# Optimization experiments

Hardware: AMD Instinct MI355X
Metric: run time of the kernel (lower is better)

Reference implementation:

```python
import jax, jax.numpy as jnp
import numpy as np

ALIGNED_H, ALIGNED_W, ALIGNED_T = 7, 7, 4
SPATIAL_SCALE, TIME_SCALE = 1.0 / 16.0, 1.0
B, C, T, H, W = 4, 256, 16, 64, 64
N_ROIS = 1200


def setup_inputs() -> dict:
    key = jax.random.key(0)
    kf, kb, kx, ky, kw, kh, kt, kd = jax.random.split(key, 8)
    features = jax.random.normal(kf, (B, C, T, H, W), dtype=jnp.float32)
    b = jax.random.randint(kb, (N_ROIS,), 0, B).astype(jnp.float32)
    # image-space boxes (1024x1024 image, stride-16 features); temporal interval in frame units
    x1 = jax.random.uniform(kx, (N_ROIS,), minval=0.0, maxval=700.0)
    y1 = jax.random.uniform(ky, (N_ROIS,), minval=0.0, maxval=700.0)
    x2 = jnp.minimum(x1 + jax.random.uniform(kw, (N_ROIS,), minval=32.0, maxval=320.0), 1023.0)
    y2 = jnp.minimum(y1 + jax.random.uniform(kh, (N_ROIS,), minval=32.0, maxval=320.0), 1023.0)
    t1 = jax.random.uniform(kt, (N_ROIS,), minval=0.0, maxval=10.0)
    t2 = jnp.minimum(t1 + jax.random.uniform(kd, (N_ROIS,), minval=2.0, maxval=6.0), 15.0)
    rois = jnp.stack([b, x1, y1, x2, y2, t1, t2], axis=1)  # [N, 7]
    return {"features": features, "rois": rois}


def _axis_samples(start, end, size, n_out):
    # classic roi_align sampling: bin = (end - start + 1) / (n_out - 1), sample at start + i*bin
    length = jnp.maximum(end - start + 1.0, 1.0)                                  # [N]
    step = length / (n_out - 1.0)
    coord = start[:, None] + step[:, None] * jnp.arange(n_out, dtype=jnp.float32)[None, :]  # [N, n_out]
    valid = (coord >= 0.0) & (coord < size)
    lo = jnp.clip(jnp.floor(coord), 0.0, size - 1.0)
    frac = coord - lo
    lo_i = lo.astype(jnp.int32)
    hi_i = jnp.minimum(lo_i + 1, size - 1)
    return lo_i, hi_i, frac, valid.astype(jnp.float32)


def roi_align_3d(features, rois, p_t, p_h, p_w, sscale, tscale):
    Bf, Cf, Tf, Hf, Wf = features.shape
    f = jnp.transpose(features, (0, 2, 3, 4, 1))  # [B,T,H,W,C] channel-last for clean gather
    bidx = rois[:, 0].astype(jnp.int32)
    x1 = rois[:, 1] * sscale
    y1 = rois[:, 2] * sscale
    x2 = rois[:, 3] * sscale
    y2 = rois[:, 4] * sscale
    t1 = rois[:, 5] * tscale
    t2 = rois[:, 6] * tscale
    tl, th, tfr, tv = _axis_samples(t1, t2, Tf, p_t)  # [N, p_t]
    yl, yh, yfr, yv = _axis_samples(y1, y2, Hf, p_h)  # [N, p_h]
    xl, xh, xfr, xv = _axis_samples(x1, x2, Wf, p_w)  # [N, p_w]
    b4 = bidx[:, None, None, None]
    out = jnp.zeros((rois.shape[0], p_t, p_h, p_w, Cf), dtype=features.dtype)
    # trilinear interpolation: sum over 8 corners
    for ti, wt in ((tl, 1.0 - tfr), (th, tfr)):
        for yi, wy in ((yl, 1.0 - yfr), (yh, yfr)):
            for xi, wx in ((xl, 1.0 - xfr), (xh, xfr)):
                v = f[b4, ti[:, :, None, None], yi[:, None, :, None], xi[:, None, None, :]]  # [N,pt,ph,pw,C]
                w = wt[:, :, None, None] * wy[:, None, :, None] * wx[:, None, None, :]
                out = out + v * w[..., None]
    # zero out-of-bounds sample points (matches CUDA kernel behavior)
    mask = tv[:, :, None, None] * yv[:, None, :, None] * xv[:, None, None, :]
    out = out * mask[..., None]
    return jnp.transpose(out, (0, 4, 1, 2, 3))  # [N, C, p_t, p_h, p_w]


def _avg_pool3d_k2s1(x):
    s = x[..., :-1, :, :] + x[..., 1:, :, :]
    s = s[..., :, :-1, :] + s[..., :, 1:, :]
    s = s[..., :, :, :-1] + s[..., :, :, 1:]
    return s * 0.125


def reference(features, rois):
    x = roi_align_3d(features, rois, ALIGNED_T + 1, ALIGNED_H + 1, ALIGNED_W + 1,
                     SPATIAL_SCALE, TIME_SCALE)
    return _avg_pool3d_k2s1(x)  # [N, C, ALIGNED_T, ALIGNED_H, ALIGNED_W]
```

## Files before the change

### kernel.cpp

```cpp
#include <hip/hip_runtime.h>

#define C_ 256
#define T_ 16
#define H_ 64
#define W_ 64
#define PT 5
#define PH 8
#define PW 8
#define OT 4
#define OH 7
#define OW 7
#define SSCALE (1.0f/16.0f)
#define TSCALE 1.0f
#define CG 32
#define LROW 66
#define NOUT (CG * OT * OH * OW)

typedef float f4v __attribute__((ext_vector_type(4)));
typedef float f2v __attribute__((ext_vector_type(2)));
typedef _Float16 h4v __attribute__((ext_vector_type(4)));
typedef _Float16 h8v __attribute__((ext_vector_type(8)));

__global__ __launch_bounds__(256) void transpose_kernel(const float* __restrict__ f,
                                                        _Float16* __restrict__ ft) {
    __shared__ _Float16 tile[64][260];
    const int THW = T_ * H_ * W_;
    int thw0 = blockIdx.x * 64;
    int b = blockIdx.y;

    int l4 = threadIdx.x & 15;
    int cr = threadIdx.x >> 4;
#pragma unroll 4
    for (int k = 0; k < 16; ++k) {
        int c = k * 16 + cr;
        const f4v* src = reinterpret_cast<const f4v*>(
            &f[((size_t)b * C_ + c) * THW + thw0 + l4 * 4]);
        f4v v = __builtin_nontemporal_load(src);
        tile[l4 * 4 + 0][c] = (_Float16)v[0];
        tile[l4 * 4 + 1][c] = (_Float16)v[1];
        tile[l4 * 4 + 2][c] = (_Float16)v[2];
        tile[l4 * 4 + 3][c] = (_Float16)v[3];
    }
    __syncthreads();

    int wv = threadIdx.x >> 6;
    int ln = threadIdx.x & 63;
    size_t orow = ((size_t)b * THW + thw0) * C_;
#pragma unroll
    for (int i = 0; i < 16; ++i) {
        int t = wv * 16 + i;
        h4v v = *reinterpret_cast<const h4v*>(&tile[t][ln * 4]);
        *reinterpret_cast<h4v*>(&ft[orow + (size_t)t * C_ + ln * 4]) = v;
    }
}

__global__ __launch_bounds__(256) void roi_kernel(const _Float16* __restrict__ ft,
                                                  const float* __restrict__ rois,
                                                  float* __restrict__ out) {
    __shared__ float scratch[NOUT];
    __shared__ float sroi[7];
    __shared__ int2 s_trow[PT]; __shared__ float2 s_twt[PT];
    __shared__ int2 s_yrow[PH]; __shared__ float2 s_ywt[PH];
    __shared__ int2 s_xoff[PW]; __shared__ float2 s_xwt[PW];

    int bid = blockIdx.x;
    int r = bid >> 3;
    int cg = bid & 7;
    int c0 = cg * CG;

    if (threadIdx.x < 7) sroi[threadIdx.x] = rois[r * 7 + threadIdx.x];
    __syncthreads();

    if (threadIdx.x < 21) {
        int i = threadIdx.x;
        float start, end, size;
        int j, n, scale;
        if (i < 5) {
            j = i; n = PT;
            start = sroi[5] * TSCALE; end = sroi[6] * TSCALE;
            size = (float)T_; scale = H_ * W_ * C_ * 2;
        } else if (i < 13) {
            j = i - 5; n = PH;
            start = sroi[2] * SSCALE; end = sroi[4] * SSCALE;
            size = (float)H_; scale = W_ * C_ * 2;
        } else {
            j = i - 13; n = PW;
            start = sroi[1] * SSCALE; end = sroi[3] * SSCALE;
            size = (float)W_; scale = C_ * 2;
        }
        float length = fmaxf(end - start + 1.0f, 1.0f);
        float step = length / (float)(n - 1);
        float coord = start + step * (float)j;
        float valid = (coord >= 0.0f && coord < size) ? 1.0f : 0.0f;
        float lo = fminf(fmaxf(floorf(coord), 0.0f), size - 1.0f);
        int lo_i = (int)lo;
        int hi_i = min(lo_i + 1, (int)size - 1);
        float fr = coord - lo;
        int2 offs; offs.x = lo_i * scale; offs.y = hi_i * scale;
        float2 wts; wts.x = (1.0f - fr) * valid; wts.y = fr * valid;
        if (i < 5)       { s_trow[j] = offs; s_twt[j] = wts; }
        else if (i < 13) { s_yrow[j] = offs; s_ywt[j] = wts; }
        else             { s_xoff[j] = offs; s_xwt[j] = wts; }
    }
    __syncthreads();

    int b = (int)sroi[0];
    int c4 = threadIdx.x & 3;
    int slot = threadIdx.x >> 2;
    const char* fb = (const char*)ft
        + ((size_t)b * (T_ * H_ * W_ * C_) + (size_t)(c0 + c4 * 8)) * 2;

    float (*buf)[LROW] = (float(*)[LROW])scratch;
    int cc = threadIdx.x & 31;
    int hh = threadIdx.x >> 5;

    float racc[OT][OW];
#pragma unroll
    for (int t = 0; t < OT; ++t)
#pragma unroll
        for (int w = 0; w < OW; ++w) racc[t][w] = 0.0f;

    int y = slot >> 3, x = slot & 7;
    int2 yr = s_yrow[y]; float2 yw = s_ywt[y];
    int2 xo = s_xoff[x]; float2 xw = s_xwt[x];

#pragma unroll
    for (int t = 0; t < PT; ++t) {
        if (t) __syncthreads();

        int2 tr = s_trow[t];
        float2 tw = s_twt[t];
        int rA = tr.x + yr.x;
        int rB = tr.x + yr.y;
        int rC = tr.y + yr.x;
        int rD = tr.y + yr.y;
        float wA = tw.x * yw.x, wB = tw.x * yw.y;
        float wC = tw.y * yw.x, wD = tw.y * yw.y;

        f4v accL = {0.f, 0.f, 0.f, 0.f};
        f4v accH = {0.f, 0.f, 0.f, 0.f};
#pragma unroll
        for (int tap = 0; tap < 8; ++tap) {
            int ro = (tap & 1) ? ((tap >> 1) == 0 ? rA : (tap >> 1) == 1 ? rB
                                  : (tap >> 1) == 2 ? rC : rD) + xo.y
                               : ((tap >> 1) == 0 ? rA : (tap >> 1) == 1 ? rB
                                  : (tap >> 1) == 2 ? rC : rD) + xo.x;
            float w = ((tap >> 1) == 0 ? wA : (tap >> 1) == 1 ? wB
                       : (tap >> 1) == 2 ? wC : wD) * ((tap & 1) ? xw.y : xw.x);
            h8v h = *(const h8v*)(fb + ro);
            f4v lo = {(float)h[0], (float)h[1], (float)h[2], (float)h[3]};
            f4v hi = {(float)h[4], (float)h[5], (float)h[6], (float)h[7]};
            accL += w * lo;
            accH += w * hi;
        }
        {
            float* col = &buf[c4 * 8][slot];
            col[0 * LROW] = accL[0];
            col[1 * LROW] = accL[1];
            col[2 * LROW] = accL[2];
            col[3 * LROW] = accL[3];
            col[4 * LROW] = accH[0];
            col[5 * LROW] = accH[1];
            col[6 * LROW] = accH[2];
            col[7 * LROW] = accH[3];
        }
        __syncthreads();

        if (hh < 7) {
            const float* p = &buf[cc][hh * 8];
            float p2[8];
#pragma unroll
            for (int x2 = 0; x2 < 4; ++x2) {
                f2v a = *(const f2v*)(p + 2 * x2);
                f2v bq = *(const f2v*)(p + 8 + 2 * x2);
                f2v s = a + bq;
                p2[2 * x2] = s[0];
                p2[2 * x2 + 1] = s[1];
            }
#pragma unroll
            for (int w = 0; w < OW; ++w) {
                float pw = p2[w] + p2[w + 1];
                if (t < OT) racc[t][w] += pw;
                if (t > 0) racc[t - 1][w] += pw;
            }
        }
    }
    __syncthreads();

    if (hh < 7) {
        int base = cc * (OT * OH * OW) + hh * OW;
#pragma unroll
        for (int t = 0; t < OT; ++t)
#pragma unroll
            for (int w = 0; w < OW; ++w)
                scratch[base + t * (OH * OW) + w] = racc[t][w] * 0.125f;
    }
    __syncthreads();

    float* outb = out + ((size_t)r * C_ + c0) * (OT * OH * OW);
    const f4v* s4 = (const f4v*)scratch;
    f4v* o4 = (f4v*)outb;
    for (int k = 0; k < 7; ++k) {
        int idx = k * 256 + threadIdx.x;
        if (idx < NOUT / 4) __builtin_nontemporal_store(s4[idx], &o4[idx]);
    }
}

__device__ __forceinline__ void axis_sample(float start, float end, float size, int n,
                                            int j, int& lo_i, int& hi_i, float& frac,
                                            float& valid) {
    float length = fmaxf(end - start + 1.0f, 1.0f);
    float step = length / (float)(n - 1);
    float coord = start + step * (float)j;
    valid = (coord >= 0.0f && coord < size) ? 1.0f : 0.0f;
    float lo = fminf(fmaxf(floorf(coord), 0.0f), size - 1.0f);
    frac = coord - lo;
    lo_i = (int)lo;
    hi_i = min(lo_i + 1, (int)size - 1);
}

__global__ void roi_direct(const float* __restrict__ f, const float* __restrict__ rois,
                           float* __restrict__ out, long long total) {
    long long idx = (long long)blockIdx.x * 256 + threadIdx.x;
    if (idx >= total) return;
    int w = (int)(idx % OW);
    long long q = idx / OW;
    int h = (int)(q % OH);
    q /= OH;
    int t = (int)(q % OT);
    q /= OT;
    int c = (int)(q % C_);
    int r = (int)(q / C_);

    float rb = rois[r * 7 + 0];
    float x1 = rois[r * 7 + 1] * SSCALE;
    float y1 = rois[r * 7 + 2] * SSCALE;
    float x2 = rois[r * 7 + 3] * SSCALE;
    float y2 = rois[r * 7 + 4] * SSCALE;
    float t1 = rois[r * 7 + 5] * TSCALE;
    float t2 = rois[r * 7 + 6] * TSCALE;
    int b = (int)rb;
    const float* fc = f + ((size_t)b * C_ + c) * (T_ * H_ * W_);

    float acc = 0.0f;
    for (int dt = 0; dt < 2; ++dt) {
        int tlo, thi; float tf, tv;
        axis_sample(t1, t2, (float)T_, PT, t + dt, tlo, thi, tf, tv);
        for (int dh = 0; dh < 2; ++dh) {
            int ylo, yhi; float yf, yv;
            axis_sample(y1, y2, (float)H_, PH, h + dh, ylo, yhi, yf, yv);
            for (int dw = 0; dw < 2; ++dw) {
                int xlo, xhi; float xf, xv;
                axis_sample(x1, x2, (float)W_, PW, w + dw, xlo, xhi, xf, xv);
                float v000 = fc[(tlo * H_ + ylo) * W_ + xlo];
                float v001 = fc[(tlo * H_ + ylo) * W_ + xhi];
                float v010 = fc[(tlo * H_ + yhi) * W_ + xlo];
                float v011 = fc[(tlo * H_ + yhi) * W_ + xhi];
                float v100 = fc[(thi * H_ + ylo) * W_ + xlo];
                float v101 = fc[(thi * H_ + ylo) * W_ + xhi];
                float v110 = fc[(thi * H_ + yhi) * W_ + xlo];
                float v111 = fc[(thi * H_ + yhi) * W_ + xhi];
                float vx00 = v000 + xf * (v001 - v000);
                float vx01 = v010 + xf * (v011 - v010);
                float vx10 = v100 + xf * (v101 - v100);
                float vx11 = v110 + xf * (v111 - v110);
                float vy0 = vx00 + yf * (vx01 - vx00);
                float vy1 = vx10 + yf * (vx11 - vx10);
                float v = vy0 + tf * (vy1 - vy0);
                acc += v * (tv * yv * xv);
            }
        }
    }
    out[idx] = acc * 0.125f;
}

extern "C" void kernel_launch(void* const* d_in, const int* in_sizes, int n_in,
                              void* d_out, int out_size, void* d_ws, size_t ws_size,
                              hipStream_t stream) {
    const float* feat = (const float*)d_in[0];
    const float* rois = (const float*)d_in[1];
    float* out = (float*)d_out;
    int nroi = in_sizes[1] / 7;
    int B = in_sizes[0] / (C_ * T_ * H_ * W_);
    size_t need = (size_t)B * T_ * H_ * W_ * C_ * sizeof(_Float16);

    if (ws_size >= need) {
        dim3 g1(T_ * H_ * W_ / 64, B);
        transpose_kernel<<<g1, 256, 0, stream>>>(feat, (_Float16*)d_ws);
        roi_kernel<<<dim3(nroi * (C_ / CG)), 256, 0, stream>>>((const _Float16*)d_ws, rois, out);
    } else {
        long long total = (long long)nroi * C_ * OT * OH * OW;
        roi_direct<<<(int)((total + 255) / 256), 256, 0, stream>>>(feat, rois, out, total);
    }
}
```

Before: 575.1 us.

## Sort ROIs by spatial Morton key and swizzle transpose shared-memory layout

Adds a single-block bitonic sort that orders ROIs by batch, Morton-coded center and time, so consecutive roi_kernel blocks touch nearby feature regions and share cache lines in L2. The transpose kernel now packs channel pairs into 32-bit words in an XOR-swizzled shared tile, replacing scattered 16-bit stores that suffered bank conflicts. This costs an extra kernel launch and a serial sort of up to 2048 keys on one workgroup.

```diff
diff --git a/kernel.cpp b/kernel.cpp
--- a/kernel.cpp
+++ b/kernel.cpp
@@ -18,28 +18,34 @@
 
 typedef float f4v __attribute__((ext_vector_type(4)));
 typedef float f2v __attribute__((ext_vector_type(2)));
-typedef _Float16 h4v __attribute__((ext_vector_type(4)));
+typedef _Float16 h2v __attribute__((ext_vector_type(2)));
 typedef _Float16 h8v __attribute__((ext_vector_type(8)));
 
 __global__ __launch_bounds__(256) void transpose_kernel(const float* __restrict__ f,
                                                         _Float16* __restrict__ ft) {
-    __shared__ _Float16 tile[64][260];
+    __shared__ unsigned tile[64 * 128];
     const int THW = T_ * H_ * W_;
     int thw0 = blockIdx.x * 64;
     int b = blockIdx.y;
-
-    int l4 = threadIdx.x & 15;
-    int cr = threadIdx.x >> 4;
-#pragma unroll 4
-    for (int k = 0; k < 16; ++k) {
-        int c = k * 16 + cr;
-        const f4v* src = reinterpret_cast<const f4v*>(
-            &f[((size_t)b * C_ + c) * THW + thw0 + l4 * 4]);
-        f4v v = __builtin_nontemporal_load(src);
-        tile[l4 * 4 + 0][c] = (_Float16)v[0];
-        tile[l4 * 4 + 1][c] = (_Float16)v[1];
-        tile[l4 * 4 + 2][c] = (_Float16)v[2];
-        tile[l4 * 4 + 3][c] = (_Float16)v[3];
+    int q = threadIdx.x & 15;
+    int cp0 = threadIdx.x >> 4;
+
+#pragma unroll
+    for (int k = 0; k < 8; ++k) {
+        int cp = k * 16 + cp0;
+        int c = cp * 2;
+        const f4v* s0 = reinterpret_cast<const f4v*>(
+            &f[((size_t)b * C_ + c) * THW + thw0 + q * 4]);
+        const f4v* s1 = reinterpret_cast<const f4v*>(
+            &f[((size_t)b * C_ + c + 1) * THW + thw0 + q * 4]);
+        f4v va = __builtin_nontemporal_load(s0);
+        f4v vb = __builtin_nontemporal_load(s1);
+#pragma unroll
+        for (int j = 0; j < 4; ++j) {
+            int row = q * 4 + j;
+            h2v hp = {(_Float16)va[j], (_Float16)vb[j]};
+            tile[row * 128 + (cp ^ (row & 30))] = __builtin_bit_cast(unsigned, hp);
+        }
     }
     __syncthreads();
 
@@ -48,14 +54,62 @@
     size_t orow = ((size_t)b * THW + thw0) * C_;
 #pragma unroll
     for (int i = 0; i < 16; ++i) {
-        int t = wv * 16 + i;
-        h4v v = *reinterpret_cast<const h4v*>(&tile[t][ln * 4]);
-        *reinterpret_cast<h4v*>(&ft[orow + (size_t)t * C_ + ln * 4]) = v;
-    }
+        int row = wv * 16 + i;
+        int s = row & 30;
+        uint2 w = *reinterpret_cast<const uint2*>(&tile[row * 128 + ((ln * 2) ^ s)]);
+        *reinterpret_cast<uint2*>(&ft[orow + (size_t)row * C_ + ln * 4]) = w;
+    }
+}
+
+__global__ __launch_bounds__(1024) void sort_rois(const float* __restrict__ rois,
+                                                  int nroi, int* __restrict__ perm) {
+    __shared__ unsigned key[2048];
+    int t = threadIdx.x;
+    if (nroi > 2048) {
+        for (int i = t; i < nroi; i += 1024) perm[i] = i;
+        return;
+    }
+    for (int i = t; i < 2048; i += 1024) {
+        unsigned k = 0x1FFFFFu;
+        if (i < nroi) {
+            const float* rp = rois + i * 7;
+            int bb = (int)rp[0];
+            float xc = (rp[1] + rp[3]) * 0.5f * SSCALE;
+            float yc = (rp[2] + rp[4]) * 0.5f * SSCALE;
+            float tc = (rp[5] + rp[6]) * 0.5f * TSCALE;
+            int xq = min(63, max(0, (int)xc));
+            int yq = min(63, max(0, (int)yc));
+            int tq = min(15, max(0, (int)tc));
+            unsigned m = 0;
+#pragma unroll
+            for (int bit = 0; bit < 6; ++bit)
+                m |= (((yq >> bit) & 1u) << (2 * bit + 1)) |
+                     (((xq >> bit) & 1u) << (2 * bit));
+            k = ((((unsigned)bb << 12) | m) << 4) | (unsigned)tq;
+        }
+        key[i] = (k << 11) | (unsigned)i;
+    }
+    __syncthreads();
+    for (int kk = 2; kk <= 2048; kk <<= 1) {
+        for (int j = kk >> 1; j > 0; j >>= 1) {
+            for (int i = t; i < 2048; i += 1024) {
+                int ixj = i ^ j;
+                if (ixj > i) {
+                    unsigned a = key[i], c = key[ixj];
+                    bool up = (i & kk) == 0;
+                    if ((a > c) == up) { key[i] = c; key[ixj] = a; }
+                }
+            }
+            __syncthreads();
+        }
+    }
+    for (int i = t; i < 2048; i += 1024)
+        if (i < nroi) perm[i] = (int)(key[i] & 0x7FFu);
 }
 
 __global__ __launch_bounds__(256) void roi_kernel(const _Float16* __restrict__ ft,
                                                   const float* __restrict__ rois,
+                                                  const int* __restrict__ perm,
                                                   float* __restrict__ out) {
     __shared__ float scratch[NOUT];
     __shared__ float sroi[7];
@@ -64,7 +118,7 @@
     __shared__ int2 s_xoff[PW]; __shared__ float2 s_xwt[PW];
 
     int bid = blockIdx.x;
-    int r = bid >> 3;
+    int r = perm[bid >> 3];
     int cg = bid & 7;
     int c0 = cg * CG;
 
@@ -282,12 +336,16 @@
     float* out = (float*)d_out;
     int nroi = in_sizes[1] / 7;
     int B = in_sizes[0] / (C_ * T_ * H_ * W_);
-    size_t need = (size_t)B * T_ * H_ * W_ * C_ * sizeof(_Float16);
-
-    if (ws_size >= need) {
+    size_t ftbytes = (size_t)B * T_ * H_ * W_ * C_ * sizeof(_Float16);
+    size_t need = ftbytes + 2048 * sizeof(int);
+
+    if (ws_size >= need && nroi >= 1) {
+        _Float16* ft = (_Float16*)d_ws;
+        int* perm = (int*)((char*)d_ws + ftbytes);
+        sort_rois<<<1, 1024, 0, stream>>>(rois, nroi, perm);
         dim3 g1(T_ * H_ * W_ / 64, B);
-        transpose_kernel<<<g1, 256, 0, stream>>>(feat, (_Float16*)d_ws);
-        roi_kernel<<<dim3(nroi * (C_ / CG)), 256, 0, stream>>>((const _Float16*)d_ws, rois, out);
+        transpose_kernel<<<g1, 256, 0, stream>>>(feat, ft);
+        roi_kernel<<<dim3(nroi * (C_ / CG)), 256, 0, stream>>>(ft, rois, perm, out);
     } else {
         long long total = (long long)nroi * C_ * OT * OH * OW;
         roi_direct<<<(int)((total + 255) / 256), 256, 0, stream>>>(feat, rois, out, total);
```

After: 525.3 us. 8.7% less time.
